# Performance work log

Hardware: AMD Instinct MI355X
Metric: run time of the kernel (lower is better)

The kernel has to match this reference:

```python
import jax, jax.numpy as jnp
import numpy as np

DN = ('NCHW', 'OIHW', 'NCHW')

def _conv(x, W, pad):
    return jax.lax.conv_general_dilated(x, W, (1, 1), [(pad, pad), (pad, pad)], dimension_numbers=DN)

def _cbs(x, W, s, b, pad):
    # Conv2d(bias=False) + folded BatchNorm (scale/bias) + SiLU
    y = _conv(x, W, pad) * s[None, :, None, None] + b[None, :, None, None]
    return y * jax.nn.sigmoid(y)

def _l2norm(x):
    n = jnp.sqrt(jnp.sum(x * x, axis=1, keepdims=True))
    return x / jnp.maximum(n, 1e-12)

def setup_inputs() -> dict:
    key = jax.random.key(0)
    ks = jax.random.split(key, 24)
    B, C, H, L, TD, NC = 16, 256, 64, 40, 768, 8
    EMB = (TD + NC * 2) // 2  # 392
    w = lambda k, sh: jax.random.normal(k, sh, jnp.float32) * 0.02
    img = jax.random.normal(ks[0], (B, C, H, H), jnp.float32)
    flang = jax.random.normal(ks[1], (B, L, TD), jnp.float32)
    lengths = jax.random.randint(ks[2], (B, 1), 5, L + 1)
    word_mask = (jnp.arange(L)[None, :] < lengths).astype(jnp.int32)
    return {
        'img': img, 'flang': flang, 'word_mask': word_mask, 'sigma_w': 0.1,
        'W1': w(ks[3], (EMB, TD)), 'b1': w(ks[4], (EMB,)),
        'W2': w(ks[5], (NC * 2, EMB)), 'b2': w(ks[6], (NC * 2,)),
        'Wv': w(ks[7], (C, C, 1, 1)), 'sv': jnp.ones((C,)), 'bv': w(ks[8], (C,)),
        'Wg': w(ks[9], (NC, NC, 1, 1)), 'sg': jnp.ones((NC,)), 'bg': w(ks[10], (NC,)),
        'Wb': w(ks[11], (NC, NC, 1, 1)), 'sb': jnp.ones((NC,)), 'bb': w(ks[12], (NC,)),
        'Wf1': w(ks[13], (C, C, 1, 1)), 'sf1': jnp.ones((C,)), 'bf1': w(ks[14], (C,)),
        'Wf2': w(ks[15], (C, C, 3, 3)), 'sf2': jnp.ones((C,)), 'bf2': w(ks[16], (C,)),
        'Wf3': w(ks[17], (C, C, 1, 1)), 'bf3': w(ks[18], (C,)),
        'Ws': w(ks[19], (NC, C, 3, 3)), 'bs': w(ks[20], (NC,)),
        'add_weight': jnp.zeros((), jnp.float32),
    }

def reference(img, flang, word_mask, sigma_w, W1, b1, W2, b2, Wv, sv, bv,
              Wg, sg, bg, Wb, sb, bb, Wf1, sf1, bf1, Wf2, sf2, bf2,
              Wf3, bf3, Ws, bs, add_weight):
    B, C, H = img.shape[0], img.shape[1], img.shape[2]
    nc = Wg.shape[0]
    map_visu = jnp.tanh(_cbs(img, Wv, sv, bv, 0))
    # ragged masked mean excluding first (CLS) and last (SEP) masked tokens
    m = word_mask.astype(jnp.float32)
    c = jnp.cumsum(m, axis=1)
    tot = c[:, -1:]
    inc = m * ((c > 1) & (c < tot)).astype(jnp.float32)  # [B,L]
    flang_avg = jnp.sum(flang * inc[:, :, None], axis=1) / jnp.sum(inc, axis=1, keepdims=True)
    map_flang = jax.nn.sigmoid((flang_avg @ W1.T + b1) @ W2.T + b2)  # [B,2*nc]
    maps = map_flang.reshape(B, nc, 2)
    sigma_x = sigma_w * H
    sig = _conv(img, Ws, 0) + bs[None, :, None, None]  # [B,nc,H-2,H-2]
    sigma_weight = jax.nn.sigmoid(jnp.mean(sig, axis=(2, 3), keepdims=True))  # [B,nc,1,1]
    sigma_y = sigma_x * sigma_weight
    yc = (maps[:, :, 0] * H).astype(jnp.int32).astype(jnp.float32)[:, :, None, None]
    xc = (maps[:, :, 1] * H).astype(jnp.int32).astype(jnp.float32)[:, :, None, None]
    gy = jnp.arange(H, dtype=jnp.float32)[None, None, :, None]
    gx = jnp.arange(H, dtype=jnp.float32)[None, None, None, :]
    weights = jnp.exp(-((gy - yc) ** 2 / (2.0 * sigma_y ** 2) + (gx - xc) ** 2 / (2.0 * sigma_x ** 2)))  # [B,nc,H,H]
    gamma = jnp.tanh(_cbs(weights, Wg, sg, bg, 0))
    beta = jnp.tanh(_cbs(weights, Wb, sb, bb, 0))
    g = jnp.mean(gamma, axis=1, keepdims=True)
    bmax = jnp.max(beta, axis=1, keepdims=True)
    v_film = _l2norm(g * map_visu + bmax)
    v_film = _cbs(v_film, Wf1, sf1, bf1, 0)
    v_film = _cbs(v_film, Wf2, sf2, bf2, 1)
    v_film = _conv(v_film, Wf3, 0) + bf3[None, :, None, None]
    aw = jnp.tanh(add_weight)
    v_add = (1.0 + aw) * img + (1.0 - aw) * v_film
    return _l2norm(v_add)
```

## Files before the change

### kernel.cpp

```cpp
#include <hip/hip_runtime.h>
#include <hip/hip_bf16.h>


#define DEVFN static __device__ __forceinline__

DEVFN float sigmoidf_(float x) { return 1.f / (1.f + expf(-x)); }
DEVFN float siluf_(float y) { return y / (1.f + __expf(-y)); }
DEVFN float tanh_fast_(float x) { return 1.f - 2.f / (__expf(2.f * x) + 1.f); }

typedef __attribute__((ext_vector_type(8))) short bf16x8;
typedef __attribute__((ext_vector_type(4))) float f32x4;

DEVFN unsigned short f2bf_(float f) {
    union { __hip_bfloat16 b; unsigned short u; } cv;
    cv.b = __float2bfloat16(f);
    return cv.u;
}
DEVFN float bf2f_(unsigned short u) {
    union { unsigned short u; __hip_bfloat16 b; } cv;
    cv.u = u;
    return __bfloat162float(cv.b);
}

DEVFN void async_cp16(const void* g, void* l) {
    __builtin_amdgcn_global_load_lds(
        (const __attribute__((address_space(1))) unsigned int*)g,
        (__attribute__((address_space(3))) unsigned int*)l, 16, 0, 0);
}

__global__ __launch_bounds__(256) void mega1_kernel(
        const float* __restrict__ Wv, const float* __restrict__ Wf1,
        const float* __restrict__ Wf3, const float* __restrict__ Wf2,
        short* __restrict__ WvB, short* __restrict__ W1B,
        short* __restrict__ W3B, short* __restrict__ WB2,
        float* __restrict__ zbuf,
        const float* __restrict__ img, float* __restrict__ S,
        const float* __restrict__ flang, const int* __restrict__ mask,
        const float* __restrict__ Wm1, const float* __restrict__ bm1,
        const float* __restrict__ Wm2, const float* __restrict__ bm2,
        float* __restrict__ ycxc) {
    __shared__ float red[9 * 256];
    __shared__ float inc[40];
    __shared__ float isum;
    __shared__ float fa[768];
    __shared__ float h[392];
    __shared__ float o[16];
    int bid = blockIdx.x, t = threadIdx.x;

    if (bid < 2560) {
        int idx = bid * 256 + t;
        if (idx < 8) zbuf[idx] = 0.f;
        if (idx < 65536) {
            int j    = idx & 7;
            int lane = (idx >> 3) & 63;
            int coT  = (idx >> 9) & 15;
            int ci32 = (idx >> 13) & 7;
            int co = coT * 16 + (lane & 15);
            int ci = ci32 * 32 + ((lane >> 4) << 3) + j;
            int src = co * 256 + ci;
            WvB[idx] = (short)f2bf_(Wv[src]);
            W1B[idx] = (short)f2bf_(Wf1[src]);
            W3B[idx] = (short)f2bf_(Wf3[src]);
        }
        int oo = idx - 65536;
        if (oo >= 0 && oo < 589824) {
            int j    = oo & 7;
            int lane = (oo >> 3) & 63;
            int coT  = (oo >> 9) & 15;
            int ci32 = (oo >> 13) & 7;
            int kk   = oo >> 16;
            int co = coT * 16 + (lane & 15);
            int ci = ci32 * 32 + ((lane >> 4) << 3) + j;
            WB2[oo] = (short)f2bf_(Wf2[(co * 256 + ci) * 9 + kk]);
        }
    } else if (bid < 6656) {
        int bc = bid - 2560;
        float s[9];
#pragma unroll
        for (int k = 0; k < 9; ++k) s[k] = 0.f;
        const float* p = img + (size_t)bc * 4096;
        for (int j = 0; j < 16; ++j) {
            int idx = t + j * 256;
            int y = idx >> 6, x = idx & 63;
            float v = p[idx];
#pragma unroll
            for (int ky = 0; ky < 3; ++ky) {
                if (y < ky || y > ky + 61) continue;
#pragma unroll
                for (int kx = 0; kx < 3; ++kx) {
                    if (x < kx || x > kx + 61) continue;
                    s[ky * 3 + kx] += v;
                }
            }
        }
#pragma unroll
        for (int k = 0; k < 9; ++k) red[k * 256 + t] = s[k];
        __syncthreads();
        for (int st = 128; st > 0; st >>= 1) {
            if (t < st) {
#pragma unroll
                for (int k = 0; k < 9; ++k) red[k * 256 + t] += red[k * 256 + t + st];
            }
            __syncthreads();
        }
        if (t < 9) S[(size_t)bc * 9 + t] = red[t * 256];
    } else {
        int b = bid - 6656;
        if (t == 0) {
            float cum[40];
            float c = 0.f;
            for (int l = 0; l < 40; ++l) { c += (float)mask[b * 40 + l]; cum[l] = c; }
            float tot = c, sm = 0.f;
            for (int l = 0; l < 40; ++l) {
                float m = (float)mask[b * 40 + l];
                float v = (cum[l] > 1.f && cum[l] < tot) ? m : 0.f;
                inc[l] = v; sm += v;
            }
            isum = sm;
        }
        __syncthreads();
        for (int d = t; d < 768; d += 256) {
            float a = 0.f;
            for (int l = 0; l < 40; ++l) a += flang[(size_t)(b * 40 + l) * 768 + d] * inc[l];
            fa[d] = a / isum;
        }
        __syncthreads();
        for (int u = t; u < 392; u += 256) {
            float a = bm1[u];
            const float* w = Wm1 + (size_t)u * 768;
            for (int k = 0; k < 768; ++k) a = fmaf(fa[k], w[k], a);
            h[u] = a;
        }
        __syncthreads();
        if (t < 16) {
            float a = bm2[t];
            const float* w = Wm2 + (size_t)t * 392;
            for (int k = 0; k < 392; ++k) a = fmaf(h[k], w[k], a);
            o[t] = sigmoidf_(a);
        }
        __syncthreads();
        if (t < 8) {
            ycxc[b * 8 + t]       = (float)(int)(o[2 * t] * 64.f);
            ycxc[128 + b * 8 + t] = (float)(int)(o[2 * t + 1] * 64.f);
        }
    }
}

__global__ __launch_bounds__(256) void f01_kernel(
        const float* __restrict__ img, const short* __restrict__ wvb,
        const short* __restrict__ w1b,
        const float* __restrict__ sv, const float* __restrict__ bv,
        const float* __restrict__ s1, const float* __restrict__ b1,
        const float* __restrict__ S, const float* __restrict__ Ws,
        const float* __restrict__ bs, const float* __restrict__ ycxc,
        const float* __restrict__ sigma_w,
        const float* __restrict__ Wg, const float* __restrict__ sg,
        const float* __restrict__ bg,
        const float* __restrict__ Wb, const float* __restrict__ sb,
        const float* __restrict__ bb,
        __hip_bfloat16* __restrict__ outB) {
    __shared__ __attribute__((aligned(16))) short lA[64 * 264];
    __shared__ float invs[64];
    __shared__ float ls_sv[256], ls_bv[256], ls_s1[256], ls_b1[256];
    __shared__ float ls_g[64], ls_bm[64];
    __shared__ float sigw8[8];
    float* red = (float*)lA;
    float* pr  = (float*)lA;
    int blk = blockIdx.x, b = blk >> 6, y = blk & 63;
    int t = threadIdx.x, w = t >> 6, lane = t & 63;
    int lx = lane & 15, koct = lane >> 4;

    ls_sv[t] = sv[t]; ls_bv[t] = bv[t];
    ls_s1[t] = s1[t]; ls_b1[t] = b1[t];

    {
        float s9[9];
        const float* Sp = S + (size_t)(b * 256 + t) * 9;
#pragma unroll
        for (int k = 0; k < 9; ++k) s9[k] = Sp[k];
#pragma unroll
        for (int co = 0; co < 8; ++co) {
            const float* wp = Ws + (size_t)(co * 256 + t) * 9;
            float a = 0.f;
#pragma unroll
            for (int k = 0; k < 9; ++k) a = fmaf(wp[k], s9[k], a);
            red[co * 256 + t] = a;
        }
        __syncthreads();
        for (int st = 128; st > 0; st >>= 1) {
            if (t < st) {
#pragma unroll
                for (int co = 0; co < 8; ++co) red[co * 256 + t] += red[co * 256 + t + st];
            }
            __syncthreads();
        }
        if (t < 8) sigw8[t] = sigmoidf_(red[t * 256] / 3844.f + bs[t]);
        __syncthreads();
    }

    if (t < 64) {
        float sx = sigma_w[0] * 64.f;
        float wv8[8];
#pragma unroll
        for (int n = 0; n < 8; ++n) {
            float yc = ycxc[b * 8 + n], xc = ycxc[128 + b * 8 + n];
            float sy = sx * sigw8[n];
            float dy = (float)y - yc, dx = (float)t - xc;
            wv8[n] = expf(-(dy * dy / (2.f * sy * sy) + dx * dx / (2.f * sx * sx)));
        }
        float gacc = 0.f, bmax = -3.4e38f;
#pragma unroll
        for (int n = 0; n < 8; ++n) {
            float a1 = 0.f, a2 = 0.f;
#pragma unroll
            for (int m = 0; m < 8; ++m) {
                a1 = fmaf(Wg[n * 8 + m], wv8[m], a1);
                a2 = fmaf(Wb[n * 8 + m], wv8[m], a2);
            }
            float ga = tanhf(siluf_(a1 * sg[n] + bg[n]));
            float be = tanhf(siluf_(a2 * sb[n] + bb[n]));
            gacc += ga;
            bmax = fmaxf(bmax, be);
        }
        ls_g[t]  = gacc * 0.125f;
        ls_bm[t] = bmax;
    }

    {
        int x = t & 63, cg = t >> 6;
        const float* ib = img + (size_t)b * 1048576 + y * 64 + x;
#pragma unroll
        for (int c8 = 0; c8 < 8; ++c8) {
            int ci0 = cg * 64 + c8 * 8;
            unsigned short r[8];
#pragma unroll
            for (int j = 0; j < 8; ++j) r[j] = f2bf_(ib[(size_t)(ci0 + j) * 4096]);
            *(uint4*)&lA[x * 264 + ci0] = *(uint4*)r;
        }
    }
    f32x4 acc[4][4];
#pragma unroll
    for (int mi = 0; mi < 4; ++mi)
#pragma unroll
        for (int ni = 0; ni < 4; ++ni) acc[mi][ni] = (f32x4){0.f, 0.f, 0.f, 0.f};
    __syncthreads();

#pragma unroll
    for (int k32 = 0; k32 < 8; ++k32) {
        const short* wp = wvb + (((k32 * 16) + w * 4) * 64 + lane) * 8;
        bf16x8 bfr[4];
#pragma unroll
        for (int ni = 0; ni < 4; ++ni) bfr[ni] = *(const bf16x8*)(wp + ni * 512);
        bf16x8 afr[4];
#pragma unroll
        for (int mi = 0; mi < 4; ++mi)
            afr[mi] = *(const bf16x8*)&lA[(mi * 16 + lx) * 264 + k32 * 32 + koct * 8];
#pragma unroll
        for (int mi = 0; mi < 4; ++mi)
#pragma unroll
            for (int ni = 0; ni < 4; ++ni)
                acc[mi][ni] = __builtin_amdgcn_mfma_f32_16x16x32_bf16(afr[mi], bfr[ni], acc[mi][ni], 0, 0, 0);
    }
    __syncthreads();

#pragma unroll
    for (int mi = 0; mi < 4; ++mi)
#pragma unroll
        for (int rr = 0; rr < 4; ++rr) {
            int x = mi * 16 + koct * 4 + rr;
            float ps = 0.f;
#pragma unroll
            for (int ni = 0; ni < 4; ++ni) {
                int co = w * 64 + ni * 16 + lx;
                float yv = fmaf(acc[mi][ni][rr], ls_sv[co], ls_bv[co]);
                float mvv = tanh_fast_(siluf_(yv));
                float v = fmaf(ls_g[x], mvv, ls_bm[x]);
                acc[mi][ni][rr] = v;
                ps += v * v;
            }
            pr[x * 64 + w * 16 + lx] = ps;
        }
    __syncthreads();
    if (t < 64) {
        float s2 = 0.f;
        for (int q = 0; q < 64; ++q) s2 += pr[t * 64 + q];
        invs[t] = 1.f / fmaxf(sqrtf(s2), 1e-12f);
    }
    __syncthreads();

#pragma unroll
    for (int mi = 0; mi < 4; ++mi)
#pragma unroll
        for (int ni = 0; ni < 4; ++ni) {
            int co = w * 64 + ni * 16 + lx;
#pragma unroll
            for (int rr = 0; rr < 4; ++rr) {
                int x = mi * 16 + koct * 4 + rr;
                lA[x * 264 + co] = (short)f2bf_(acc[mi][ni][rr] * invs[x]);
            }
        }
#pragma unroll
    for (int mi = 0; mi < 4; ++mi)
#pragma unroll
        for (int ni = 0; ni < 4; ++ni) acc[mi][ni] = (f32x4){0.f, 0.f, 0.f, 0.f};
    __syncthreads();

#pragma unroll
    for (int k32 = 0; k32 < 8; ++k32) {
        const short* wp = w1b + (((k32 * 16) + w * 4) * 64 + lane) * 8;
        bf16x8 bfr[4];
#pragma unroll
        for (int ni = 0; ni < 4; ++ni) bfr[ni] = *(const bf16x8*)(wp + ni * 512);
        bf16x8 afr[4];
#pragma unroll
        for (int mi = 0; mi < 4; ++mi)
            afr[mi] = *(const bf16x8*)&lA[(mi * 16 + lx) * 264 + k32 * 32 + koct * 8];
#pragma unroll
        for (int mi = 0; mi < 4; ++mi)
#pragma unroll
            for (int ni = 0; ni < 4; ++ni)
                acc[mi][ni] = __builtin_amdgcn_mfma_f32_16x16x32_bf16(afr[mi], bfr[ni], acc[mi][ni], 0, 0, 0);
    }
    __syncthreads();

#pragma unroll
    for (int mi = 0; mi < 4; ++mi)
#pragma unroll
        for (int ni = 0; ni < 4; ++ni) {
            int co = w * 64 + ni * 16 + lx;
#pragma unroll
            for (int rr = 0; rr < 4; ++rr) {
                int x = mi * 16 + koct * 4 + rr;
                float yv = fmaf(acc[mi][ni][rr], ls_s1[co], ls_b1[co]);
                lA[x * 264 + co] = (short)f2bf_(siluf_(yv));
            }
        }
    __syncthreads();
    unsigned short* og = (unsigned short*)outB + (size_t)(b * 64 + y) * 16384;
#pragma unroll
    for (int it = 0; it < 8; ++it) {
        int e8 = t + it * 256;
        int x2 = e8 >> 5, c8 = e8 & 31;
        *(uint4*)(og + e8 * 8) = *(uint4*)&lA[x2 * 264 + c8 * 8];
    }
}

DEVFN void stage_chunk(const unsigned short* __restrict__ xg, short* ldsbuf,
                       const unsigned short* __restrict__ zbuf, int cc, int y0, int t) {
#pragma unroll
    for (int p = 0; p < 10; ++p) {
        int slot = t + p * 256;
        if (slot < 2376) {
            int r = slot / 594;
            int rem = slot - r * 594;
            int xp = rem / 9;
            int oct = rem - xp * 9;
            int ys = y0 + r - 1, xs = xp - 1;
            bool valid = (oct < 8) && (ys >= 0) && (ys < 64) && (xs >= 0) && (xs < 64);
            const unsigned short* gp = valid ? (xg + ((ys * 64 + xs) * 256 + cc * 64 + oct * 8))
                                             : zbuf;
            async_cp16(gp, ldsbuf + slot * 8);
        }
    }
}

__global__ __launch_bounds__(256, 2) void c3f_kernel(const __hip_bfloat16* __restrict__ xin,
                                                     const short* __restrict__ wb,
                                                     const float* __restrict__ sc,
                                                     const float* __restrict__ bi,
                                                     const float* __restrict__ zbufF,
                                                     const short* __restrict__ w3b,
                                                     const float* __restrict__ bf3,
                                                     const float* __restrict__ img,
                                                     const float* __restrict__ addw,
                                                     float* __restrict__ outF) {
    __shared__ __attribute__((aligned(16))) short lds[2][19008];
    __shared__ float pr2[256];
    __shared__ float invs[64];
    __shared__ float ls_b3[256];
    int blk = blockIdx.x;
    int b = blk >> 5, y0 = (blk & 31) * 2;
    int t = threadIdx.x;
    int w = t >> 6, lane = t & 63;
    int lx = lane & 15, koct = lane >> 4;
    const unsigned short* xg = (const unsigned short*)xin + (size_t)b * 1048576;
    const unsigned short* zbuf = (const unsigned short*)zbufF;
    ls_b3[t] = bf3[t];

    f32x4 acc[8][4];
#pragma unroll
    for (int mi = 0; mi < 8; ++mi)
#pragma unroll
        for (int ni = 0; ni < 4; ++ni) acc[mi][ni] = (f32x4){0.f, 0.f, 0.f, 0.f};

    stage_chunk(xg, lds[0], zbuf, 0, y0, t);
    __syncthreads();

    for (int cc = 0; cc < 4; ++cc) {
        short* cur = lds[cc & 1];
        if (cc < 3) stage_chunk(xg, lds[(cc + 1) & 1], zbuf, cc + 1, y0, t);
        for (int kk = 0; kk < 9; ++kk) {
            int ky = kk / 3, kx = kk - ky * 3;
#pragma unroll
            for (int k32 = 0; k32 < 2; ++k32) {
                const short* wp = wb + ((((kk * 8 + cc * 2 + k32) * 16) + w * 4) * 64 + lane) * 8;
                bf16x8 bfr[4];
#pragma unroll
                for (int ni = 0; ni < 4; ++ni)
                    bfr[ni] = *(const bf16x8*)(wp + ni * 512);
                bf16x8 afr[8];
#pragma unroll
                for (int mi = 0; mi < 8; ++mi) {
                    int row = mi >> 2, xb = (mi & 3) * 16;
                    afr[mi] = *(const bf16x8*)&cur[((row + ky) * 66 + xb + lx + kx) * 72 + k32 * 32 + koct * 8];
                }
#pragma unroll
                for (int mi = 0; mi < 8; ++mi)
#pragma unroll
                    for (int ni = 0; ni < 4; ++ni)
                        acc[mi][ni] = __builtin_amdgcn_mfma_f32_16x16x32_bf16(afr[mi], bfr[ni], acc[mi][ni], 0, 0, 0);
            }
        }
        __syncthreads();
    }

    float aw = tanhf(addw[0]);
    float ca = 1.f + aw, cb = 1.f - aw;
    short* ep  = &lds[0][0];
    short* wst = &lds[1][0];
#pragma unroll
    for (int r2 = 0; r2 < 2; ++r2) {
#pragma unroll
        for (int mi4 = 0; mi4 < 4; ++mi4) {
            int mi = r2 * 4 + mi4;
#pragma unroll
            for (int ni = 0; ni < 4; ++ni) {
                int co = w * 64 + ni * 16 + lx;
                float s = sc[co], bb2 = bi[co];
#pragma unroll
                for (int rr = 0; rr < 4; ++rr) {
                    int x = mi4 * 16 + koct * 4 + rr;
                    float yv = fmaf(acc[mi][ni][rr], s, bb2);
                    ep[x * 264 + co] = (short)f2bf_(siluf_(yv));
                }
            }
        }
        __syncthreads();
        f32x4 acc2[4][4];
#pragma unroll
        for (int mi = 0; mi < 4; ++mi)
#pragma unroll
            for (int ni = 0; ni < 4; ++ni) acc2[mi][ni] = (f32x4){0.f, 0.f, 0.f, 0.f};
#pragma unroll
        for (int k32 = 0; k32 < 8; ++k32) {
            const short* wp = w3b + (((k32 * 16) + w * 4) * 64 + lane) * 8;
            bf16x8 bfr[4];
#pragma unroll
            for (int ni = 0; ni < 4; ++ni) bfr[ni] = *(const bf16x8*)(wp + ni * 512);
            bf16x8 afr[4];
#pragma unroll
            for (int mi = 0; mi < 4; ++mi)
                afr[mi] = *(const bf16x8*)&ep[(mi * 16 + lx) * 264 + k32 * 32 + koct * 8];
#pragma unroll
            for (int mi = 0; mi < 4; ++mi)
#pragma unroll
                for (int ni = 0; ni < 4; ++ni)
                    acc2[mi][ni] = __builtin_amdgcn_mfma_f32_16x16x32_bf16(afr[mi], bfr[ni], acc2[mi][ni], 0, 0, 0);
        }
#pragma unroll
        for (int mi = 0; mi < 4; ++mi)
#pragma unroll
            for (int ni = 0; ni < 4; ++ni) {
                int co = w * 64 + ni * 16 + lx;
                float b3 = ls_b3[co];
#pragma unroll
                for (int rr = 0; rr < 4; ++rr) {
                    int x = mi * 16 + koct * 4 + rr;
                    wst[co * 66 + x] = (short)f2bf_(acc2[mi][ni][rr] + b3);
                }
            }
        __syncthreads();
        int x = t & 63, cg = t >> 6;
        const float* ip = img + (size_t)b * 1048576 + (size_t)(y0 + r2) * 64 + x;
        float ss = 0.f;
#pragma unroll 8
        for (int j = 0; j < 64; ++j) {
            int co = cg * 64 + j;
            float v = fmaf(cb, bf2f_((unsigned short)wst[co * 66 + x]), ca * ip[(size_t)co * 4096]);
            ss += v * v;
        }
        pr2[cg * 64 + x] = ss;
        __syncthreads();
        if (t < 64)
            invs[t] = 1.f / fmaxf(sqrtf(pr2[t] + pr2[64 + t] + pr2[128 + t] + pr2[192 + t]), 1e-12f);
        __syncthreads();
        float iv = invs[x];
        float* op = outF + (size_t)b * 1048576 + (size_t)(y0 + r2) * 64 + x;
#pragma unroll 8
        for (int j = 0; j < 64; ++j) {
            int co = cg * 64 + j;
            float v = fmaf(cb, bf2f_((unsigned short)wst[co * 66 + x]), ca * ip[(size_t)co * 4096]);
            op[(size_t)co * 4096] = v * iv;
        }
        __syncthreads();
    }
}

extern "C" void kernel_launch(void* const* d_in, const int* in_sizes, int n_in,
                              void* d_out, int out_size, void* d_ws, size_t ws_size,
                              hipStream_t stream) {
    const float* img     = (const float*)d_in[0];
    const float* flang   = (const float*)d_in[1];
    const int*   wmask   = (const int*)d_in[2];
    const float* sigma_w = (const float*)d_in[3];
    const float* W1      = (const float*)d_in[4];
    const float* b1      = (const float*)d_in[5];
    const float* W2      = (const float*)d_in[6];
    const float* b2      = (const float*)d_in[7];
    const float* Wv      = (const float*)d_in[8];
    const float* sv      = (const float*)d_in[9];
    const float* bv      = (const float*)d_in[10];
    const float* Wg      = (const float*)d_in[11];
    const float* sg      = (const float*)d_in[12];
    const float* bg      = (const float*)d_in[13];
    const float* Wb      = (const float*)d_in[14];
    const float* sb      = (const float*)d_in[15];
    const float* bb      = (const float*)d_in[16];
    const float* Wf1     = (const float*)d_in[17];
    const float* sf1     = (const float*)d_in[18];
    const float* bf1     = (const float*)d_in[19];
    const float* Wf2     = (const float*)d_in[20];
    const float* sf2     = (const float*)d_in[21];
    const float* bf2     = (const float*)d_in[22];
    const float* Wf3     = (const float*)d_in[23];
    const float* bf3     = (const float*)d_in[24];
    const float* Ws      = (const float*)d_in[25];
    const float* bs      = (const float*)d_in[26];
    const float* addw    = (const float*)d_in[27];
    float* out = (float*)d_out;
    float* ws  = (float*)d_ws;

    short* WvB  = (short*)ws;
    short* W1B  = (short*)(ws + 32768);
    short* W3B  = (short*)(ws + 65536);
    short* WB2  = (short*)(ws + 98304);
    float* ycxc = ws + 393216;
    float* S    = ws + 393472;
    float* zbuf = ws + 430336;
    __hip_bfloat16* bufB = (__hip_bfloat16*)(ws + 430352);

    mega1_kernel<<<6672, 256, 0, stream>>>(Wv, Wf1, Wf3, Wf2, WvB, W1B, W3B, WB2, zbuf,
                                           img, S, flang, wmask, W1, b1, W2, b2, ycxc);
    f01_kernel<<<1024, 256, 0, stream>>>(img, WvB, W1B, sv, bv, sf1, bf1,
                                         S, Ws, bs, ycxc, sigma_w,
                                         Wg, sg, bg, Wb, sb, bb, bufB);
    c3f_kernel<<<512, 256, 0, stream>>>(bufB, WB2, sf2, bf2, zbuf, W3B, bf3, img, addw, out);
}
```

Baseline: 415.4 us.

## Restructure prologue kernel: wave-level reductions, vectorized loads, reordered block roles

The first kernel is reorganised. Each wave now computes one image channel's 3x3 window sums using float4 loads and shuffle reductions, replacing the per-block shared-memory tree reduction. The language MLP now uses wave-cooperative float4 dot products instead of one thread per output row, and its blocks are scheduled first so the serial chain starts early. Weight conversion handles four elements per thread, which shrinks the grid from 6672 to 1680 blocks. This cuts launch, sync and latency overhead in the prologue, at the cost of more complex edge-mask arithmetic.

```diff
diff --git a/kernel.cpp b/kernel.cpp
--- a/kernel.cpp
+++ b/kernel.cpp
@@ -27,6 +27,10 @@
         (const __attribute__((address_space(1))) unsigned int*)g,
         (__attribute__((address_space(3))) unsigned int*)l, 16, 0, 0);
 }
+
+#define M1_LANG_END 16
+#define M1_WSUM_END 1040
+#define M1_GRID     1680
 
 __global__ __launch_bounds__(256) void mega1_kernel(
         const float* __restrict__ Wv, const float* __restrict__ Wf1,
@@ -39,109 +43,143 @@
         const float* __restrict__ Wm1, const float* __restrict__ bm1,
         const float* __restrict__ Wm2, const float* __restrict__ bm2,
         float* __restrict__ ycxc) {
-    __shared__ float red[9 * 256];
+    __shared__ int   mlds[40];
     __shared__ float inc[40];
     __shared__ float isum;
-    __shared__ float fa[768];
+    __shared__ __attribute__((aligned(16))) float fa[768];
     __shared__ float h[392];
-    __shared__ float o[16];
+    __shared__ float o16[16];
     int bid = blockIdx.x, t = threadIdx.x;
-
-    if (bid < 2560) {
-        int idx = bid * 256 + t;
-        if (idx < 8) zbuf[idx] = 0.f;
-        if (idx < 65536) {
-            int j    = idx & 7;
-            int lane = (idx >> 3) & 63;
-            int coT  = (idx >> 9) & 15;
-            int ci32 = (idx >> 13) & 7;
-            int co = coT * 16 + (lane & 15);
-            int ci = ci32 * 32 + ((lane >> 4) << 3) + j;
-            int src = co * 256 + ci;
-            WvB[idx] = (short)f2bf_(Wv[src]);
-            W1B[idx] = (short)f2bf_(Wf1[src]);
-            W3B[idx] = (short)f2bf_(Wf3[src]);
-        }
-        int oo = idx - 65536;
-        if (oo >= 0 && oo < 589824) {
-            int j    = oo & 7;
-            int lane = (oo >> 3) & 63;
-            int coT  = (oo >> 9) & 15;
-            int ci32 = (oo >> 13) & 7;
-            int kk   = oo >> 16;
-            int co = coT * 16 + (lane & 15);
-            int ci = ci32 * 32 + ((lane >> 4) << 3) + j;
-            WB2[oo] = (short)f2bf_(Wf2[(co * 256 + ci) * 9 + kk]);
-        }
-    } else if (bid < 6656) {
-        int bc = bid - 2560;
+    int w = t >> 6, lane = t & 63;
+
+    if (bid < M1_LANG_END) {
+        int b = bid;
+        if (t < 40) mlds[t] = mask[b * 40 + t];
+        __syncthreads();
+        if (t == 0) {
+            float cum = 0.f;
+            float tot = 0.f;
+            for (int l = 0; l < 40; ++l) tot += (float)mlds[l];
+            float sm = 0.f;
+            for (int l = 0; l < 40; ++l) {
+                float m = (float)mlds[l];
+                cum += m;
+                float v = (cum > 1.f && cum < tot) ? m : 0.f;
+                inc[l] = v; sm += v;
+            }
+            isum = sm;
+        }
+        __syncthreads();
+        {
+            float rinv = 1.f / isum;
+            for (int d = t; d < 768; d += 256) {
+                float a = 0.f;
+                const float* fp = flang + (size_t)(b * 40) * 768 + d;
+                for (int l = 0; l < 40; ++l) a = fmaf(fp[(size_t)l * 768], inc[l], a);
+                fa[d] = a * rinv;
+            }
+        }
+        __syncthreads();
+        {
+            const float4* W14 = (const float4*)Wm1;
+            const float4* fa4 = (const float4*)fa;
+            for (int u = w; u < 392; u += 4) {
+                float a = 0.f;
+#pragma unroll
+                for (int j = 0; j < 3; ++j) {
+                    float4 wv = W14[(size_t)u * 192 + j * 64 + lane];
+                    float4 fv = fa4[j * 64 + lane];
+                    a = fmaf(wv.x, fv.x, a);
+                    a = fmaf(wv.y, fv.y, a);
+                    a = fmaf(wv.z, fv.z, a);
+                    a = fmaf(wv.w, fv.w, a);
+                }
+#pragma unroll
+                for (int m = 32; m; m >>= 1) a += __shfl_xor(a, m);
+                if (lane == 0) h[u] = a + bm1[u];
+            }
+        }
+        __syncthreads();
+        {
+#pragma unroll
+            for (int q = 0; q < 4; ++q) {
+                int u2 = w * 4 + q;
+                float a = 0.f;
+#pragma unroll
+                for (int j = 0; j < 7; ++j) {
+                    int k = j * 64 + lane;
+                    if (k < 392) a = fmaf(h[k], Wm2[(size_t)u2 * 392 + k], a);
+                }
+#pragma unroll
+                for (int m = 32; m; m >>= 1) a += __shfl_xor(a, m);
+                if (lane == 0) o16[u2] = sigmoidf_(a + bm2[u2]);
+            }
+        }
+        __syncthreads();
+        if (t < 8) {
+            ycxc[b * 8 + t]       = (float)(int)(o16[2 * t] * 64.f);
+            ycxc[128 + b * 8 + t] = (float)(int)(o16[2 * t + 1] * 64.f);
+        }
+    } else if (bid < M1_WSUM_END) {
+        int bc = (bid - M1_LANG_END) * 4 + w;
+        const float4* p4 = (const float4*)(img + (size_t)bc * 4096);
+        int lx2 = lane & 15;
         float s[9];
 #pragma unroll
         for (int k = 0; k < 9; ++k) s[k] = 0.f;
-        const float* p = img + (size_t)bc * 4096;
-        for (int j = 0; j < 16; ++j) {
-            int idx = t + j * 256;
-            int y = idx >> 6, x = idx & 63;
-            float v = p[idx];
-#pragma unroll
-            for (int ky = 0; ky < 3; ++ky) {
-                if (y < ky || y > ky + 61) continue;
-#pragma unroll
-                for (int kx = 0; kx < 3; ++kx) {
-                    if (x < kx || x > kx + 61) continue;
-                    s[ky * 3 + kx] += v;
-                }
-            }
-        }
-#pragma unroll
-        for (int k = 0; k < 9; ++k) red[k * 256 + t] = s[k];
-        __syncthreads();
-        for (int st = 128; st > 0; st >>= 1) {
-            if (t < st) {
-#pragma unroll
-                for (int k = 0; k < 9; ++k) red[k * 256 + t] += red[k * 256 + t + st];
-            }
-            __syncthreads();
-        }
-        if (t < 9) S[(size_t)bc * 9 + t] = red[t * 256];
+#pragma unroll
+        for (int i = 0; i < 16; ++i) {
+            float4 v = p4[lane + i * 64];
+            int y = (lane >> 4) + 4 * i;
+            float sum4 = v.x + v.y + v.z + v.w;
+            float p0 = (lx2 == 15) ? (v.x + v.y) : sum4;
+            float p1 = sum4 - ((lx2 == 0) ? v.x : 0.f)
+                            - ((lx2 == 15) ? v.w : 0.f);
+            float p2 = (lx2 == 0) ? (v.z + v.w) : sum4;
+            float ym0 = (y <= 61) ? 1.f : 0.f;
+            float ym1 = (y >= 1 && y <= 62) ? 1.f : 0.f;
+            float ym2 = (y >= 2) ? 1.f : 0.f;
+            s[0] = fmaf(ym0, p0, s[0]); s[1] = fmaf(ym0, p1, s[1]); s[2] = fmaf(ym0, p2, s[2]);
+            s[3] = fmaf(ym1, p0, s[3]); s[4] = fmaf(ym1, p1, s[4]); s[5] = fmaf(ym1, p2, s[5]);
+            s[6] = fmaf(ym2, p0, s[6]); s[7] = fmaf(ym2, p1, s[7]); s[8] = fmaf(ym2, p2, s[8]);
+        }
+#pragma unroll
+        for (int m = 32; m; m >>= 1)
+#pragma unroll
+            for (int k = 0; k < 9; ++k) s[k] += __shfl_xor(s[k], m);
+        if (lane == 0) {
+#pragma unroll
+            for (int k = 0; k < 9; ++k) S[(size_t)bc * 9 + k] = s[k];
+        }
     } else {
-        int b = bid - 6656;
-        if (t == 0) {
-            float cum[40];
-            float c = 0.f;
-            for (int l = 0; l < 40; ++l) { c += (float)mask[b * 40 + l]; cum[l] = c; }
-            float tot = c, sm = 0.f;
-            for (int l = 0; l < 40; ++l) {
-                float m = (float)mask[b * 40 + l];
-                float v = (cum[l] > 1.f && cum[l] < tot) ? m : 0.f;
-                inc[l] = v; sm += v;
-            }
-            isum = sm;
-        }
-        __syncthreads();
-        for (int d = t; d < 768; d += 256) {
-            float a = 0.f;
-            for (int l = 0; l < 40; ++l) a += flang[(size_t)(b * 40 + l) * 768 + d] * inc[l];
-            fa[d] = a / isum;
-        }
-        __syncthreads();
-        for (int u = t; u < 392; u += 256) {
-            float a = bm1[u];
-            const float* w = Wm1 + (size_t)u * 768;
-            for (int k = 0; k < 768; ++k) a = fmaf(fa[k], w[k], a);
-            h[u] = a;
-        }
-        __syncthreads();
-        if (t < 16) {
-            float a = bm2[t];
-            const float* w = Wm2 + (size_t)t * 392;
-            for (int k = 0; k < 392; ++k) a = fmaf(h[k], w[k], a);
-            o[t] = sigmoidf_(a);
-        }
-        __syncthreads();
-        if (t < 8) {
-            ycxc[b * 8 + t]       = (float)(int)(o[2 * t] * 64.f);
-            ycxc[128 + b * 8 + t] = (float)(int)(o[2 * t + 1] * 64.f);
+        int base = (bid - M1_WSUM_END) * 1024;
+#pragma unroll
+        for (int i = 0; i < 4; ++i) {
+            int idx = base + i * 256 + t;
+            if (idx < 8) zbuf[idx] = 0.f;
+            if (idx < 65536) {
+                int j    = idx & 7;
+                int ln   = (idx >> 3) & 63;
+                int coT  = (idx >> 9) & 15;
+                int ci32 = (idx >> 13) & 7;
+                int co = coT * 16 + (ln & 15);
+                int ci = ci32 * 32 + ((ln >> 4) << 3) + j;
+                int src = co * 256 + ci;
+                WvB[idx] = (short)f2bf_(Wv[src]);
+                W1B[idx] = (short)f2bf_(Wf1[src]);
+                W3B[idx] = (short)f2bf_(Wf3[src]);
+            }
+            int oo = idx - 65536;
+            if (oo >= 0 && oo < 589824) {
+                int j    = oo & 7;
+                int ln   = (oo >> 3) & 63;
+                int coT  = (oo >> 9) & 15;
+                int ci32 = (oo >> 13) & 7;
+                int kk   = oo >> 16;
+                int co = coT * 16 + (ln & 15);
+                int ci = ci32 * 32 + ((ln >> 4) << 3) + j;
+                WB2[oo] = (short)f2bf_(Wf2[(co * 256 + ci) * 9 + kk]);
+            }
         }
     }
 }
@@ -549,8 +587,8 @@
     float* zbuf = ws + 430336;
     __hip_bfloat16* bufB = (__hip_bfloat16*)(ws + 430352);
 
-    mega1_kernel<<<6672, 256, 0, stream>>>(Wv, Wf1, Wf3, Wf2, WvB, W1B, W3B, WB2, zbuf,
-                                           img, S, flang, wmask, W1, b1, W2, b2, ycxc);
+    mega1_kernel<<<M1_GRID, 256, 0, stream>>>(Wv, Wf1, Wf3, Wf2, WvB, W1B, W3B, WB2, zbuf,
+                                              img, S, flang, wmask, W1, b1, W2, b2, ycxc);
     f01_kernel<<<1024, 256, 0, stream>>>(img, WvB, W1B, sv, bv, sf1, bf1,
                                          S, Ws, bs, ycxc, sigma_w,
                                          Wg, sg, bg, Wb, sb, bb, bufB);
```

After: 407.9 us. Within noise of the previous version (-1.8%).
